# Optimization experiments

Hardware: AMD Instinct MI355X
Metric: run time of the kernel (lower is better)

Reference implementation:

```python
import jax, jax.numpy as jnp
import numpy as np

D_MODEL = 1024
N_HEADS = 16
HEAD_DIM = D_MODEL // N_HEADS
SEQ = 2048
BATCH = 2
ROPE_BASE = 10000.0


def rope_cos_sin(seq_len, dim, dtype=jnp.float32):
    inv_freq = 1.0 / (ROPE_BASE ** (jnp.arange(0, dim, 2, dtype=jnp.float32) / dim))
    pos = jnp.arange(seq_len, dtype=jnp.float32)
    freqs = jnp.outer(pos, inv_freq)              # [S, dim/2]
    emb = jnp.concatenate([freqs, freqs], axis=-1)  # [S, dim]
    return jnp.cos(emb).astype(dtype), jnp.sin(emb).astype(dtype)


def rotate_half(x):
    x1, x2 = jnp.split(x, 2, axis=-1)
    return jnp.concatenate([-x2, x1], axis=-1)


def setup_inputs() -> dict:
    key = jax.random.key(0)
    kx, kq, kk, kv, ko = jax.random.split(key, 5)
    x = jax.random.normal(kx, (BATCH, SEQ, D_MODEL), dtype=jnp.float32)
    # causal boolean mask, broadcastable to [B, H, S, S]
    attn_mask = jnp.tril(jnp.ones((SEQ, SEQ), dtype=bool))[None, None]
    s = 1.0 / np.sqrt(D_MODEL)
    Wq = jax.random.normal(kq, (D_MODEL, D_MODEL), dtype=jnp.float32) * s
    Wk = jax.random.normal(kk, (D_MODEL, D_MODEL), dtype=jnp.float32) * s
    Wv = jax.random.normal(kv, (D_MODEL, D_MODEL), dtype=jnp.float32) * s
    Wo = jax.random.normal(ko, (D_MODEL, D_MODEL), dtype=jnp.float32) * s
    return {"x": x, "attn_mask": attn_mask, "Wq": Wq, "Wk": Wk, "Wv": Wv, "Wo": Wo}


def reference(x, attn_mask, Wq, Wk, Wv, Wo):
    B, S, _ = x.shape
    dtype = x.dtype
    # projections (nn.Linear: x @ W.T)
    def split_heads(t):
        return t.reshape(B, S, N_HEADS, HEAD_DIM).transpose(0, 2, 1, 3)  # [B,H,S,Dh]
    q = split_heads(x @ Wq.T)
    k = split_heads(x @ Wk.T)
    v = split_heads(x @ Wv.T)
    # RoPE
    cos, sin = rope_cos_sin(S, HEAD_DIM, dtype)  # [S, Dh]
    cos = cos[None, None]
    sin = sin[None, None]
    q = q * cos + rotate_half(q) * sin
    k = k * cos + rotate_half(k) * sin
    # float mask: 0 where True, finfo.min where False
    neg = jnp.finfo(dtype).min
    float_mask = jnp.where(attn_mask, jnp.zeros((), dtype), jnp.full((), neg, dtype))
    # scaled dot product attention
    scale = 1.0 / np.sqrt(HEAD_DIM)
    scores = jnp.einsum("bhqd,bhkd->bhqk", q, k) * scale + float_mask
    attn = jax.nn.softmax(scores, axis=-1)
    out = jnp.einsum("bhqk,bhkd->bhqd", attn, v)  # [B,H,S,Dh]
    out = out.transpose(0, 2, 1, 3).reshape(B, S, D_MODEL)
    return out @ Wo.T
```

## Files before the change

kernel.cpp:

```cpp
#include <hip/hip_runtime.h>
#include <hip/hip_bf16.h>
#include <math.h>

typedef unsigned short ushort_t;
typedef __attribute__((ext_vector_type(8))) short short8;
typedef __attribute__((ext_vector_type(4))) float f32x4;

#define D_MODEL 1024
#define SEQ     2048
#define NH      16
#define HD      64
#define BATCH   2
#define M_TOTAL (BATCH * SEQ)
#define SCL     0.18033688f
#define HSZ     4194304

__device__ __forceinline__ ushort_t f2bf(float f) {
    __hip_bfloat16 h = __float2bfloat16(f);
    ushort_t u;
    __builtin_memcpy(&u, &h, 2);
    return u;
}
__device__ __forceinline__ unsigned pack2(float a, float b) {
    __hip_bfloat162 h = __float22bfloat162_rn(make_float2(a, b));
    unsigned u;
    __builtin_memcpy(&u, &h, 4);
    return u;
}
__device__ __forceinline__ float fexp2(float x) { return __builtin_amdgcn_exp2f(x); }

typedef const __attribute__((address_space(1))) void* gp_t;
typedef __attribute__((address_space(3))) void* lp_t;
__device__ __forceinline__ void cp16(const void* g, void* l) {
    __builtin_amdgcn_global_load_lds((gp_t)g, (lp_t)l, 16, 0, 0);
}

__global__ __launch_bounds__(256) void prep(
    const float* __restrict__ x,
    const float* __restrict__ w0, const float* __restrict__ w1,
    const float* __restrict__ w2, const float* __restrict__ w3,
    ushort_t* __restrict__ xb, ushort_t* __restrict__ wb,
    float2* __restrict__ tab)
{
    int bid = blockIdx.x;
    if (bid < 4096) {
        size_t e = ((size_t)bid * 256 + threadIdx.x) * 8;
        const float* src;
        ushort_t* dst;
        size_t off;
        if (e < (size_t)HSZ) {
            src = x; dst = xb; off = e;
        } else {
            size_t r = e - HSZ;
            int j = (int)(r >> 20);
            off = r & 1048575u;
            src = (j == 0) ? w0 : (j == 1) ? w1 : (j == 2) ? w2 : w3;
            dst = wb + ((size_t)j << 20);
        }
        float4 a = *(const float4*)&src[off];
        float4 b = *(const float4*)&src[off + 4];
        uint4 u;
        u.x = pack2(a.x, a.y);
        u.y = pack2(a.z, a.w);
        u.z = pack2(b.x, b.y);
        u.w = pack2(b.z, b.w);
        *(uint4*)&dst[off] = u;
    } else {
        int idx = (bid - 4096) * 256 + threadIdx.x;
        int i = idx & 31, s = idx >> 5;
        float invf = powf(10000.0f, -(float)(2 * i) * (1.0f / 64.0f));
        float fr = (float)s * invf;
        float sn, cs;
        sincosf(fr, &sn, &cs);
        tab[idx] = make_float2(cs, sn);
    }
}

template <int OMODE>
__global__ __launch_bounds__(256) void gemm_k(
    const ushort_t* __restrict__ A,
    const ushort_t* __restrict__ W0, const ushort_t* __restrict__ W1,
    const ushort_t* __restrict__ W2,
    void* __restrict__ D0v, void* __restrict__ D1v, void* __restrict__ D2v,
    const float2* __restrict__ tab)
{
    constexpr int BN = (OMODE == 1) ? 64 : 128;
    constexpr int NJ = BN / 32;
    __shared__ ushort_t As[2][128 * 32];
    __shared__ ushort_t Bs[2][BN * 32];
    const int K = D_MODEL;
    const int t = threadIdx.x;
    const int l = t & 63, w = t >> 6;
    const int wm = (w & 1) * 64, wn = (w >> 1) * (BN / 2);
    const int r15 = l & 15, q4 = l >> 4;

    const int bid = blockIdx.x;
    const int xcd = bid & 7, loc = bid >> 3;
    const int mt = (xcd >> 1) * 8 + (loc & 7);
    int nt, z;
    if (OMODE == 0) {
        int rest = loc >> 3;
        nt = (xcd & 1) * 4 + (rest & 3);
        z  = rest >> 2;
    } else {
        nt = (xcd & 1) * 8 + (loc >> 3);
        z  = 0;
    }
    const int m0 = mt * 128, n0 = nt * BN;
    const ushort_t* Wp = (z == 0) ? W0 : (z == 1 ? W1 : W2);
    void* Dp           = (z == 0) ? D0v : (z == 1 ? D1v : D2v);

    f32x4 acc[4][NJ];
#pragma unroll
    for (int i = 0; i < 4; ++i)
#pragma unroll
        for (int j = 0; j < NJ; ++j) acc[i][j] = (f32x4){0.f, 0.f, 0.f, 0.f};

    const int i0 = t, i1 = t + 256;
    const int ro0 = i0 >> 2, c0 = ((i0 & 3) - (ro0 >> 1)) & 3;
    const int ro1 = i1 >> 2, c1 = ((i1 & 3) - (ro1 >> 1)) & 3;

    auto stage = [&](int k0, int buf) {
        cp16(&A [(size_t)(m0 + ro0) * K + k0 + c0 * 8], &As[buf][i0 * 8]);
        cp16(&A [(size_t)(m0 + ro1) * K + k0 + c1 * 8], &As[buf][i1 * 8]);
        cp16(&Wp[(size_t)(n0 + ro0) * K + k0 + c0 * 8], &Bs[buf][i0 * 8]);
        if constexpr (BN == 128)
            cp16(&Wp[(size_t)(n0 + ro1) * K + k0 + c1 * 8], &Bs[buf][i1 * 8]);
    };

    stage(0, 0);
    for (int ki = 0; ki < K / 32; ++ki) {
        __syncthreads();
        if (ki < K / 32 - 1) stage((ki + 1) * 32, (ki + 1) & 1);
        const int buf = ki & 1;
        short8 af[4], bfr[NJ];
#pragma unroll
        for (int i = 0; i < 4; ++i) {
            int R = wm + 16 * i + r15;
            af[i] = *(const short8*)&As[buf][(R * 4 + ((q4 + (R >> 1)) & 3)) * 8];
        }
#pragma unroll
        for (int j = 0; j < NJ; ++j) {
            int R = wn + 16 * j + r15;
            bfr[j] = *(const short8*)&Bs[buf][(R * 4 + ((q4 + (R >> 1)) & 3)) * 8];
        }
#pragma unroll
        for (int i = 0; i < 4; ++i)
#pragma unroll
            for (int j = 0; j < NJ; ++j)
                acc[i][j] = __builtin_amdgcn_mfma_f32_16x16x32_bf16(
                    af[i], bfr[j], acc[i][j], 0, 0, 0);
    }

    if (OMODE == 1) {
        float* Dst = (float*)Dp;
#pragma unroll
        for (int i = 0; i < 4; ++i)
#pragma unroll
            for (int j = 0; j < NJ; ++j)
#pragma unroll
                for (int r = 0; r < 4; ++r) {
                    int row = m0 + wm + 16 * i + q4 * 4 + r;
                    int col = n0 + wn + 16 * j + r15;
                    Dst[(size_t)row * D_MODEL + col] = acc[i][j][r];
                }
    } else if (z < 2) {
        ushort_t* Dst = (ushort_t*)Dp;
        const float scl = (z == 0) ? SCL : 1.0f;
#pragma unroll
        for (int i = 0; i < 4; ++i) {
#pragma unroll
            for (int r = 0; r < 4; ++r) {
                int row = m0 + wm + 16 * i + q4 * 4 + r;
                int b = row >> 11, s = row & (SEQ - 1);
                const float2* trow = &tab[s * 32];
#pragma unroll
                for (int j = 0; j < 2; ++j) {
                    int col = n0 + wn + 16 * j + r15;
                    int h = col >> 6, f = 16 * j + r15;
                    float2 csn = trow[f];
                    float cs = csn.x * scl, sn = csn.y * scl;
                    float lo = acc[i][j][r], hi = acc[i][j + 2][r];
                    size_t o = (((size_t)(b * NH + h)) * SEQ + s) * HD + f;
                    Dst[o]      = f2bf(lo * cs - hi * sn);
                    Dst[o + 32] = f2bf(hi * cs + lo * sn);
                }
            }
        }
    } else {
        ushort_t* Dst = (ushort_t*)Dp;
#pragma unroll
        for (int i = 0; i < 4; ++i)
#pragma unroll
            for (int j = 0; j < 4; ++j)
#pragma unroll
                for (int r = 0; r < 4; ++r) {
                    int row = m0 + wm + 16 * i + q4 * 4 + r;
                    int col = n0 + wn + 16 * j + r15;
                    int b = row >> 11, s = row & (SEQ - 1);
                    int h = col >> 6, d = col & (HD - 1);
                    size_t o = (((size_t)(b * NH + h)) * HD + d) * SEQ + s;
                    Dst[o] = f2bf(acc[i][j][r]);
                }
    }
}

__global__ __launch_bounds__(256, 3) void attn_fused(
    const ushort_t* __restrict__ Qw, const ushort_t* __restrict__ Kw,
    const ushort_t* __restrict__ Vt, ushort_t* __restrict__ Ow)
{
    __shared__ __align__(16) ushort_t Kl[2][64 * 64];
    __shared__ __align__(16) ushort_t Vl[2][64 * 64];
    __shared__ __align__(16) ushort_t Ps[4][16 * 72];

    const int t = threadIdx.x;
    const int l = t & 63, w = t >> 6;
    const int r15 = l & 15, q4 = l >> 4;
    const int bid = blockIdx.x;
    const int loc = bid >> 3;
    const int bh  = (bid & 7) * 4 + (loc & 3);
    const int s   = 31 - (loc >> 2);
    const int m   = s * 4 + w;
    const size_t baseQK = (size_t)bh * SEQ * HD;
    const size_t baseV  = (size_t)bh * HD * SEQ;

    const int L0 = t, L1 = t + 256;
    const int r0 = L0 >> 3, c0 = (L0 & 7) ^ (r0 & 7);
    const int r1 = L1 >> 3, c1 = (L1 & 7) ^ (r1 & 7);

    const ushort_t* qp = &Qw[baseQK + (size_t)(m * 16 + r15) * HD + q4 * 8];
    short8 qf0 = *(const short8*)qp;
    short8 qf1 = *(const short8*)(qp + 32);

    f32x4 oacc[4];
    float part[4];
#pragma unroll
    for (int nb = 0; nb < 4; ++nb) oacc[nb] = (f32x4){0.f, 0.f, 0.f, 0.f};
#pragma unroll
    for (int r = 0; r < 4; ++r) part[r] = 0.f;

    const int ig0 = m * 16 + q4 * 4;
    ushort_t* ps = &Ps[w][0];

    auto stage = [&](int jt, int buf) {
        cp16(&Kw[baseQK + (size_t)(jt * 64 + r0) * HD + c0 * 8], &Kl[buf][L0 * 8]);
        cp16(&Kw[baseQK + (size_t)(jt * 64 + r1) * HD + c1 * 8], &Kl[buf][L1 * 8]);
        cp16(&Vt[baseV + (size_t)r0 * SEQ + jt * 64 + c0 * 8],   &Vl[buf][L0 * 8]);
        cp16(&Vt[baseV + (size_t)r1 * SEQ + jt * 64 + c1 * 8],   &Vl[buf][L1 * 8]);
    };

    auto process = [&](int jt, int buf) {
        f32x4 sc[4];
#pragma unroll
        for (int nb = 0; nb < 4; ++nb) {
            int R  = nb * 16 + r15;
            int a0 = R * 8 + (q4 ^ (R & 7));
            int a1 = R * 8 + ((q4 + 4) ^ (R & 7));
            short8 kb0 = *(const short8*)&Kl[buf][a0 * 8];
            short8 kb1 = *(const short8*)&Kl[buf][a1 * 8];
            f32x4 zz = (f32x4){0.f, 0.f, 0.f, 0.f};
            zz = __builtin_amdgcn_mfma_f32_16x16x32_bf16(qf0, kb0, zz, 0, 0, 0);
            sc[nb] = __builtin_amdgcn_mfma_f32_16x16x32_bf16(qf1, kb1, zz, 0, 0, 0);
        }
        const bool diag = (jt == s);
#pragma unroll
        for (int r = 0; r < 4; ++r) {
            float p0 = fexp2(sc[0][r]), p1 = fexp2(sc[1][r]);
            float p2 = fexp2(sc[2][r]), p3 = fexp2(sc[3][r]);
            if (diag) {
                int qg = ig0 + r, jb = jt * 64 + r15;
                p0 = (jb      <= qg) ? p0 : 0.f;
                p1 = (jb + 16 <= qg) ? p1 : 0.f;
                p2 = (jb + 32 <= qg) ? p2 : 0.f;
                p3 = (jb + 48 <= qg) ? p3 : 0.f;
            }
            part[r] += (p0 + p1) + (p2 + p3);
            int ro = (q4 * 4 + r) * 72 + r15;
            ps[ro]      = f2bf(p0);
            ps[ro + 16] = f2bf(p1);
            ps[ro + 32] = f2bf(p2);
            ps[ro + 48] = f2bf(p3);
        }
        short8 pf0 = *(const short8*)&ps[r15 * 72 + q4 * 8];
        short8 pf1 = *(const short8*)&ps[r15 * 72 + q4 * 8 + 32];
#pragma unroll
        for (int nb = 0; nb < 4; ++nb) {
            int R  = nb * 16 + r15;
            int a0 = R * 8 + (q4 ^ (R & 7));
            int a1 = R * 8 + ((q4 + 4) ^ (R & 7));
            short8 vb0 = *(const short8*)&Vl[buf][a0 * 8];
            short8 vb1 = *(const short8*)&Vl[buf][a1 * 8];
            f32x4 o = __builtin_amdgcn_mfma_f32_16x16x32_bf16(pf0, vb0, oacc[nb], 0, 0, 0);
            oacc[nb] = __builtin_amdgcn_mfma_f32_16x16x32_bf16(pf1, vb1, o, 0, 0, 0);
        }
    };

    stage(0, 0);
    for (int jt = 0; jt <= s; ++jt) {
        __syncthreads();
        if (jt < s) stage(jt + 1, (jt + 1) & 1);
        process(jt, jt & 1);
    }

    float lsum[4];
#pragma unroll
    for (int r = 0; r < 4; ++r) {
        float rs = part[r];
#pragma unroll
        for (int off = 1; off < 16; off <<= 1)
            rs += __shfl_xor(rs, off, 64);
        lsum[r] = 1.0f / rs;
    }

    const int b = bh >> 4, h = bh & 15;
#pragma unroll
    for (int nb = 0; nb < 4; ++nb) {
#pragma unroll
        for (int r = 0; r < 4; ++r) {
            int sg = m * 16 + q4 * 4 + r;
            int d  = nb * 16 + r15;
            Ow[((size_t)(b * SEQ + sg)) * D_MODEL + h * HD + d] =
                f2bf(oacc[nb][r] * lsum[r]);
        }
    }
}

extern "C" void kernel_launch(void* const* d_in, const int* in_sizes, int n_in,
                              void* d_out, int out_size, void* d_ws, size_t ws_size,
                              hipStream_t stream)
{
    const float* x  = (const float*)d_in[0];
    const float* Wq = (const float*)d_in[2];
    const float* Wk = (const float*)d_in[3];
    const float* Wv = (const float*)d_in[4];
    const float* Wo = (const float*)d_in[5];

    ushort_t* qw = (ushort_t*)d_ws;
    ushort_t* kw = qw + HSZ;
    ushort_t* vt = kw + HSZ;
    ushort_t* xb = vt + HSZ;
    ushort_t* aw = xb;
    ushort_t* wb = xb + HSZ;
    float2*  tab = (float2*)(wb + HSZ);

    prep<<<4096 + 256, 256, 0, stream>>>(x, Wq, Wk, Wv, Wo, xb, wb, tab);
    gemm_k<0><<<768, 256, 0, stream>>>(
        xb, wb, wb + (1 << 20), wb + (2 << 20), qw, kw, vt, tab);
    attn_fused<<<1024, 256, 0, stream>>>(qw, kw, vt, aw);
    gemm_k<1><<<512, 256, 0, stream>>>(
        aw, wb + (3 << 20), nullptr, nullptr,
        (float*)d_out, nullptr, nullptr, nullptr);
}
```

Before: 190.9 us.

## Triple-buffer GEMM k-loop with explicit vmcnt waits and vectorize V-transpose stores

The projection GEMM moves from a double-buffered LDS pipeline to a three-stage ring that prefetches two k-tiles ahead. It uses explicit s_waitcnt vmcnt counts and raw s_barrier calls in place of __syncthreads, so global loads can overlap the MFMA work better. Separately, the transposed V output now writes four consecutive bf16 values as one 8-byte store instead of four scalar 2-byte stores. The costs are more shared memory per block, which may lower occupancy, and a second barrier per iteration. The hand-tuned vmcnt values depend on how many cp16 loads each stage issues.

```diff
diff --git a/kernel.cpp b/kernel.cpp
--- a/kernel.cpp
+++ b/kernel.cpp
@@ -86,8 +86,9 @@
 {
     constexpr int BN = (OMODE == 1) ? 64 : 128;
     constexpr int NJ = BN / 32;
-    __shared__ ushort_t As[2][128 * 32];
-    __shared__ ushort_t Bs[2][BN * 32];
+    constexpr int NK = D_MODEL / 32;
+    __shared__ ushort_t As[3][128 * 32];
+    __shared__ ushort_t Bs[3][BN * 32];
     const int K = D_MODEL;
     const int t = threadIdx.x;
     const int l = t & 63, w = t >> 6;
@@ -129,20 +130,30 @@
     };
 
     stage(0, 0);
-    for (int ki = 0; ki < K / 32; ++ki) {
-        __syncthreads();
-        if (ki < K / 32 - 1) stage((ki + 1) * 32, (ki + 1) & 1);
-        const int buf = ki & 1;
+    stage(32, 1);
+    int cur = 0;
+    for (int ki = 0; ki < NK; ++ki) {
+        if (ki < NK - 1) {
+            if constexpr (OMODE == 1) asm volatile("s_waitcnt vmcnt(3)" ::: "memory");
+            else                      asm volatile("s_waitcnt vmcnt(4)" ::: "memory");
+        } else {
+            asm volatile("s_waitcnt vmcnt(0)" ::: "memory");
+        }
+        __builtin_amdgcn_s_barrier();
+        if (ki + 2 < NK) {
+            int st = cur + 2; if (st >= 3) st -= 3;
+            stage((ki + 2) * 32, st);
+        }
         short8 af[4], bfr[NJ];
 #pragma unroll
         for (int i = 0; i < 4; ++i) {
             int R = wm + 16 * i + r15;
-            af[i] = *(const short8*)&As[buf][(R * 4 + ((q4 + (R >> 1)) & 3)) * 8];
+            af[i] = *(const short8*)&As[cur][(R * 4 + ((q4 + (R >> 1)) & 3)) * 8];
         }
 #pragma unroll
         for (int j = 0; j < NJ; ++j) {
             int R = wn + 16 * j + r15;
-            bfr[j] = *(const short8*)&Bs[buf][(R * 4 + ((q4 + (R >> 1)) & 3)) * 8];
+            bfr[j] = *(const short8*)&Bs[cur][(R * 4 + ((q4 + (R >> 1)) & 3)) * 8];
         }
 #pragma unroll
         for (int i = 0; i < 4; ++i)
@@ -150,6 +161,9 @@
             for (int j = 0; j < NJ; ++j)
                 acc[i][j] = __builtin_amdgcn_mfma_f32_16x16x32_bf16(
                     af[i], bfr[j], acc[i][j], 0, 0, 0);
+        asm volatile("s_waitcnt lgkmcnt(0)" ::: "memory");
+        __builtin_amdgcn_s_barrier();
+        cur = (cur == 2) ? 0 : cur + 1;
     }
 
     if (OMODE == 1) {
@@ -192,16 +206,17 @@
 #pragma unroll
         for (int i = 0; i < 4; ++i)
 #pragma unroll
-            for (int j = 0; j < 4; ++j)
-#pragma unroll
-                for (int r = 0; r < 4; ++r) {
-                    int row = m0 + wm + 16 * i + q4 * 4 + r;
-                    int col = n0 + wn + 16 * j + r15;
-                    int b = row >> 11, s = row & (SEQ - 1);
-                    int h = col >> 6, d = col & (HD - 1);
-                    size_t o = (((size_t)(b * NH + h)) * HD + d) * SEQ + s;
-                    Dst[o] = f2bf(acc[i][j][r]);
-                }
+            for (int j = 0; j < 4; ++j) {
+                int row0 = m0 + wm + 16 * i + q4 * 4;
+                int col  = n0 + wn + 16 * j + r15;
+                int b = row0 >> 11, s0 = row0 & (SEQ - 1);
+                int h = col >> 6, d = col & (HD - 1);
+                size_t o = (((size_t)(b * NH + h)) * HD + d) * SEQ + s0;
+                uint2 u;
+                u.x = pack2(acc[i][j][0], acc[i][j][1]);
+                u.y = pack2(acc[i][j][2], acc[i][j][3]);
+                *(uint2*)&Dst[o] = u;
+            }
     }
 }
 
```

After: 187.0 us. 1.02x faster.
